# Performance work log

Hardware: AMD Instinct MI355X
Metric: run time of the kernel (lower is better)

The kernel has to match this reference:

```python
import jax, jax.numpy as jnp
import numpy as np

N_NODES, EMB, HID, HEADS, E = 50000, 128, 64, 3, 800000


def setup_inputs() -> dict:
    key = jax.random.key(0)
    ks = jax.random.split(key, 12)
    HC = HEADS * HID
    return {
        "edge_index": jax.random.randint(ks[0], (2, E), 0, N_NODES),
        "edge_attr": jax.random.uniform(ks[1], (E, 1), dtype=jnp.float32),
        "path_emb": jax.random.normal(ks[2], (N_NODES, EMB), dtype=jnp.float32) * (2.0 / EMB) ** 0.5,
        "sim_w": jnp.ones((1,), dtype=jnp.float32),
        "Wl": jax.random.normal(ks[3], (HC, EMB), dtype=jnp.float32) / np.sqrt(EMB),
        "bl": jnp.zeros((HC,), dtype=jnp.float32),
        "Wr": jax.random.normal(ks[4], (HC, EMB), dtype=jnp.float32) / np.sqrt(EMB),
        "br": jnp.zeros((HC,), dtype=jnp.float32),
        "We": jax.random.normal(ks[5], (HC, 1), dtype=jnp.float32),
        "att": jax.random.normal(ks[6], (1, HEADS, HID), dtype=jnp.float32) / np.sqrt(HID),
        "bias_gnn": jnp.zeros((HID,), dtype=jnp.float32),
        "Wout": jax.random.normal(ks[7], (1, HID), dtype=jnp.float32) / np.sqrt(HID),
        "bout": jnp.zeros((1,), dtype=jnp.float32),
    }


def reference(edge_index, edge_attr, path_emb, sim_w, Wl, bl, Wr, br, We, att, bias_gnn, Wout, bout):
    # SimFusionModule: softmax-weighted combination over sim channels -> [E, 1]
    w = jax.nn.softmax(sim_w, axis=0)
    fused = (edge_attr * w).sum(axis=1, keepdims=True)  # [E,1]

    # GATv2Conv (concat=False, no self loops, edge_dim=1)
    xl = (path_emb @ Wl.T + bl).reshape(-1, HEADS, HID)  # source transform [N,H,C]
    xr = (path_emb @ Wr.T + br).reshape(-1, HEADS, HID)  # target transform [N,H,C]
    src, dst = edge_index[0], edge_index[1]
    xj = xl[src]                                          # [E,H,C] gathered source
    xi = xr[dst]                                          # [E,H,C] gathered target
    ef = (fused @ We.T).reshape(-1, HEADS, HID)           # [E,H,C] edge features
    m = xj + xi + ef
    a = (jax.nn.leaky_relu(m, 0.2) * att).sum(-1)         # [E,H] attention logits

    # segment softmax over incoming edges of each destination node
    amax = jax.ops.segment_max(a, dst, num_segments=N_NODES)
    aexp = jnp.exp(a - amax[dst])
    asum = jax.ops.segment_sum(aexp, dst, num_segments=N_NODES)
    alpha = aexp / asum[dst]                              # [E,H]

    out = jax.ops.segment_sum(alpha[:, :, None] * xj, dst, num_segments=N_NODES)  # [N,H,C]
    out = out.mean(axis=1) + bias_gnn                     # concat=False -> head mean, + bias

    scores = (out @ Wout.T + bout).squeeze()              # [N]
    return jax.nn.softmax(scores, axis=0)
```

## Files before the change

### kernel.cpp

```cpp
#include <hip/hip_runtime.h>
#include <cfloat>
#include <cmath>

#define NHEADS 3
#define HIDC   64
#define HCC    192
#define EMBC   128
#define WCOLS  384
#define CAP    1280
#define SCH    2048
#define SPLIT  2

typedef unsigned short bhalf;
typedef __fp16 half_t;
typedef __attribute__((ext_vector_type(2))) __fp16 h2;
typedef __attribute__((ext_vector_type(8))) short bf16x8;
typedef __attribute__((ext_vector_type(4))) float f32x4;
typedef __attribute__((ext_vector_type(2))) float f32x2;

__device__ __forceinline__ unsigned f2bf(float f) {
  unsigned u = __float_as_uint(f);
  return (u + 0x7FFFu + ((u >> 16) & 1u)) >> 16;
}
__device__ __forceinline__ unsigned h2bits(h2 v) {
  union { h2 h; unsigned u; } cv; cv.h = v; return cv.u;
}

__global__ __launch_bounds__(256) void prep_kernel(
    const float* __restrict__ Wl, const float* __restrict__ Wr,
    const float* __restrict__ bl, const float* __restrict__ br,
    const float* __restrict__ We, const float* __restrict__ att,
    bhalf* __restrict__ Wb, float* __restrict__ bfl,
    unsigned* __restrict__ weh, unsigned* __restrict__ atth,
    unsigned* __restrict__ cur, float* __restrict__ sumexp, int NB)
{
  const int BASE = WCOLS * EMBC;
  int gt = blockIdx.x * 256 + threadIdx.x;
  if (gt < BASE) {
    int c = gt >> 7, k = gt & 127;
    float v = (c < HCC) ? Wl[c * EMBC + k] : Wr[(c - HCC) * EMBC + k];
    Wb[gt] = (bhalf)f2bf(v);
  } else if (gt < BASE + 384) {
    int c = gt - BASE;
    bfl[c] = (c < HCC) ? bl[c] : br[c - HCC];
  } else if (gt < BASE + 480) {
    int i = gt - BASE - 384;
    weh[i] = h2bits(__builtin_amdgcn_cvt_pkrtz(16.f * We[2 * i], 16.f * We[2 * i + 1]));
  } else if (gt < BASE + 576) {
    int i = gt - BASE - 480;
    atth[i] = h2bits(__builtin_amdgcn_cvt_pkrtz(att[2 * i] * (1.f / 16.f),
                                                att[2 * i + 1] * (1.f / 16.f)));
  } else if (gt < BASE + 576 + NB) {
    int b = gt - BASE - 576;
    cur[b * 16] = (unsigned)(b * CAP);
  } else if (gt == BASE + 576 + NB) {
    *sumexp = 0.f;
  }
}

__global__ __launch_bounds__(256, 4) void gemmscatter_kernel(
    const float* __restrict__ pe, const bhalf* __restrict__ Wb,
    const float* __restrict__ bfl, const float* __restrict__ Wout,
    unsigned char* __restrict__ xl8, unsigned char* __restrict__ xr8,
    float* __restrict__ pj, int N,
    const int* __restrict__ ei, const float* __restrict__ ea,
    uint2* __restrict__ eb, unsigned* __restrict__ cur, int E, int NSC)
{
  __shared__ union {
    bhalf Ws[192 * 64];
    struct { unsigned lh[800]; unsigned lbase[800]; } s;
  } sm;
  const int tid = threadIdx.x;

  if ((int)blockIdx.x < NSC) {
    const int base = blockIdx.x * SCH;
    for (int i = tid; i < 800; i += 256) sm.s.lh[i] = 0;
    __syncthreads();
    unsigned packed[SCH / 256];
    #pragma unroll
    for (int i = 0; i < SCH / 256; ++i) {
      int e = base + i * 256 + tid;
      packed[i] = 0xFFFFFFFFu;
      if (e < E) {
        unsigned dst = (unsigned)ei[E + e];
        unsigned r = atomicAdd(&sm.s.lh[dst >> 6], 1u);
        packed[i] = dst | (r << 16);
      }
    }
    __syncthreads();
    for (int i = tid; i < 800; i += 256) {
      unsigned c = sm.s.lh[i];
      sm.s.lbase[i] = c ? atomicAdd(&cur[i * 16], c) : 0u;
    }
    __syncthreads();
    #pragma unroll
    for (int i = 0; i < SCH / 256; ++i) {
      int e = base + i * 256 + tid;
      if (e < E) {
        unsigned pk = packed[i];
        unsigned dst = pk & 0xFFFFu;
        unsigned slot = sm.s.lbase[dst >> 6] + (pk >> 16);
        uint2 rec;
        rec.x = (unsigned)ei[e] | (dst << 16);
        rec.y = __float_as_uint(ea[e]);
        eb[slot] = rec;
      }
    }
  } else {
    const int bid  = blockIdx.x - NSC;
    const int w    = tid >> 6;
    const int lane = tid & 63;
    const int m    = lane & 15;
    const int q    = lane >> 4;
    const int nb   = bid >> 1;
    const int half = bid & 1;
    const int node = nb * 64 + w * 16 + m;
    const size_t prow = (size_t)(node < N ? node : N - 1) * EMBC;

    bf16x8 pfrag[4];
    #pragma unroll
    for (int kt = 0; kt < 4; ++kt) {
      const float* p = pe + prow + kt * 32 + q * 8;
      float4 x = *(const float4*)p;
      float4 y = *(const float4*)(p + 4);
      union { bf16x8 v; unsigned u[4]; } uu;
      uu.u[0] = (__float_as_uint(x.x) >> 16) | (__float_as_uint(x.y) & 0xFFFF0000u);
      uu.u[1] = (__float_as_uint(x.z) >> 16) | (__float_as_uint(x.w) & 0xFFFF0000u);
      uu.u[2] = (__float_as_uint(y.x) >> 16) | (__float_as_uint(y.y) & 0xFFFF0000u);
      uu.u[3] = (__float_as_uint(y.z) >> 16) | (__float_as_uint(y.w) & 0xFFFF0000u);
      pfrag[kt] = uu.v;
    }

    f32x4 acc[12];
    #pragma unroll
    for (int t = 0; t < 12; ++t) acc[t] = (f32x4){0.f, 0.f, 0.f, 0.f};

    for (int kh = 0; kh < 2; ++kh) {
      __syncthreads();
      for (int f = tid; f < 192 * 8; f += 256) {
        int cc = f >> 3, s = f & 7;
        uint4 v = *(const uint4*)(Wb + (size_t)(half * HCC + cc) * EMBC + kh * 64 + s * 8);
        *(uint4*)(sm.Ws + cc * 64 + ((s ^ (cc & 7)) * 8)) = v;
      }
      __syncthreads();
      #pragma unroll
      for (int kt2 = 0; kt2 < 2; ++kt2) {
        #pragma unroll
        for (int t = 0; t < 12; ++t) {
          bf16x8 wf = *(const bf16x8*)(sm.Ws + (t * 16 + m) * 64 + (((kt2 << 2) + q) ^ (m & 7)) * 8);
          acc[t] = __builtin_amdgcn_mfma_f32_16x16x32_bf16(wf, pfrag[kh * 2 + kt2], acc[t], 0, 0, 0);
        }
      }
    }

    float4 wo4[4];
    #pragma unroll
    for (int tt = 0; tt < 4; ++tt)
      wo4[tt] = *(const float4*)(Wout + tt * 16 + q * 4);
    float pjp[3] = {0.f, 0.f, 0.f};
    unsigned char* xo = half ? xr8 : xl8;
    #pragma unroll
    for (int t = 0; t < 12; ++t) {
      int col = t * 16 + q * 4;
      float4 b = *(const float4*)(bfl + half * HCC + col);
      float r0 = acc[t][0] + b.x;
      float r1 = acc[t][1] + b.y;
      float r2 = acc[t][2] + b.z;
      float r3 = acc[t][3] + b.w;
      if (half == 0) {
        float4 wo = wo4[t & 3];
        pjp[t >> 2] += r0 * wo.x + r1 * wo.y + r2 * wo.z + r3 * wo.w;
      }
      if (node < N) {
        int p = 0;
        p = __builtin_amdgcn_cvt_pk_fp8_f32(16.f * r0, 16.f * r1, p, false);
        p = __builtin_amdgcn_cvt_pk_fp8_f32(16.f * r2, 16.f * r3, p, true);
        *(unsigned*)(xo + (size_t)node * HCC + col) = (unsigned)p;
      }
    }
    if (half == 0) {
      #pragma unroll
      for (int h = 0; h < 3; ++h) {
        pjp[h] += __shfl_xor(pjp[h], 16);
        pjp[h] += __shfl_xor(pjp[h], 32);
      }
      if (q == 0 && node < N) {
        pj[node * 3 + 0] = pjp[0];
        pj[node * 3 + 1] = pjp[1];
        pj[node * 3 + 2] = pjp[2];
      }
    }
  }
}

#define EPG 5
#define GPW 4
#define WCHUNK (EPG * GPW)
__global__ __launch_bounds__(256, 4) void edge_kernel(
    const uint2* __restrict__ eb,
    const unsigned char* __restrict__ xl8, const unsigned char* __restrict__ xr8,
    const float* __restrict__ pj, const unsigned* __restrict__ weh,
    const unsigned* __restrict__ atth, const unsigned* __restrict__ cur,
    float* __restrict__ pfacc, int N)
{
  __shared__ float facc[64][8];
  const int tid  = threadIdx.x;
  const int w    = tid >> 6;
  const int lane = tid & 63;
  const int j = lane / 12;
  const int c = lane % 12;
  const bool act = lane < 60;
  const int cc = act ? c : 0;
  const int blk    = blockIdx.x;
  const int bucket = blk >> 1;
  const int sl     = blk & 1;
  const int start = bucket * CAP;
  const int end   = (int)cur[bucket * 16];

  for (int i = tid; i < 512; i += 256) ((float*)facc)[i] = 0.f;

  union U8 { uint4 u[2]; h2 h[8]; };
  U8 we, at;
  we.u[0] = *(const uint4*)(weh + cc * 8);
  we.u[1] = *(const uint4*)(weh + cc * 8 + 4);
  at.u[0] = *(const uint4*)(atth + cc * 8);
  at.u[1] = *(const uint4*)(atth + cc * 8 + 4);
  const h2 c02 = {(__fp16)0.2f, (__fp16)0.2f};
  __syncthreads();

  const int gw = sl * 4 + w;
  const int wstart = start + gw * WCHUNK;
  uint2 rec[GPW];
  #pragma unroll
  for (int g = 0; g < GPW; ++g) {
    int e = wstart + g * EPG + j;
    rec[g] = eb[e < end ? e : start];
  }

  for (int cb = wstart; cb < end; cb += 8 * WCHUNK) {
    int srcs[GPW], dsts[GPW]; float eavs[GPW];
    #pragma unroll
    for (int g = 0; g < GPW; ++g) {
      srcs[g] = (int)(rec[g].x & 0xFFFFu);
      dsts[g] = (int)(rec[g].x >> 16);
      eavs[g] = __uint_as_float(rec[g].y);
    }
    uint4 ul[GPW], ur[GPW]; float pjv[GPW];
    #pragma unroll
    for (int g = 0; g < GPW; ++g)
      ul[g] = *(const uint4*)(xl8 + (size_t)srcs[g] * HCC + cc * 16);
    #pragma unroll
    for (int g = 0; g < GPW; ++g)
      ur[g] = *(const uint4*)(xr8 + (size_t)dsts[g] * HCC + cc * 16);
    #pragma unroll
    for (int g = 0; g < GPW; ++g)
      pjv[g] = pj[srcs[g] * 3 + (c >> 2)];

    int nxt = cb + 8 * WCHUNK;
    #pragma unroll
    for (int g = 0; g < GPW; ++g) {
      int e = nxt + g * EPG + j;
      rec[g] = eb[(e < end) ? e : start];
    }

    #pragma unroll
    for (int g = 0; g < GPW; ++g) {
      const unsigned* ulp = &ul[g].x;
      const unsigned* urp = &ur[g].x;
      h2 eav2 = __builtin_amdgcn_cvt_pkrtz(eavs[g], eavs[g]);
      float sc = 0.f;
      #pragma unroll
      for (int i = 0; i < 4; ++i) {
        f32x2 la = __builtin_amdgcn_cvt_pk_f32_fp8(ulp[i], false);
        f32x2 lb = __builtin_amdgcn_cvt_pk_f32_fp8(ulp[i], true);
        f32x2 ra = __builtin_amdgcn_cvt_pk_f32_fp8(urp[i], false);
        f32x2 rb = __builtin_amdgcn_cvt_pk_f32_fp8(urp[i], true);
        h2 l0 = __builtin_amdgcn_cvt_pkrtz(la.x, la.y);
        h2 l1 = __builtin_amdgcn_cvt_pkrtz(lb.x, lb.y);
        h2 r0 = __builtin_amdgcn_cvt_pkrtz(ra.x, ra.y);
        h2 r1 = __builtin_amdgcn_cvt_pkrtz(rb.x, rb.y);
        h2 m0 = l0 + r0 + eav2 * we.h[2 * i];
        h2 m1 = l1 + r1 + eav2 * we.h[2 * i + 1];
        h2 q0 = __builtin_elementwise_max(m0, m0 * c02);
        h2 q1 = __builtin_elementwise_max(m1, m1 * c02);
        sc = __builtin_amdgcn_fdot2(q0, at.h[2 * i], sc, false);
        sc = __builtin_amdgcn_fdot2(q1, at.h[2 * i + 1], sc, false);
      }
      sc += __shfl_xor(sc, 1);
      sc += __shfl_xor(sc, 2);
      bool ve = act && (cb + g * EPG + j < end);
      if (ve && (c & 3) == 0) {
        int h = c >> 2;
        int ld = dsts[g] & 63;
        float ex = __expf(sc);
        atomicAdd(&facc[ld][h], ex);
        atomicAdd(&facc[ld][3 + h], ex * pjv[g]);
      }
    }
  }
  __syncthreads();

  for (int i = tid; i < 512; i += 256)
    pfacc[(size_t)blk * 512 + i] = ((float*)facc)[i];
}

__global__ __launch_bounds__(256) void finalize_kernel(
    const float* __restrict__ pfacc, float* __restrict__ sumexp,
    float* __restrict__ out, int N)
{
  int n = blockIdx.x * 256 + threadIdx.x;
  int t = threadIdx.x;
  float e = 0.f;
  if (n < N) {
    int bucket = n >> 6, ld = n & 63;
    float a0 = 0.f, a1 = 0.f, a2 = 0.f, m0 = 0.f, m1 = 0.f, m2 = 0.f;
    #pragma unroll
    for (int s = 0; s < SPLIT; ++s) {
      const float* p = pfacc + ((size_t)(bucket * SPLIT + s) * 512) + ld * 8;
      a0 += p[0]; a1 += p[1]; a2 += p[2];
      m0 += p[3]; m1 += p[4]; m2 += p[5];
    }
    float accs = 0.f;
    if (a0 > 0.f) accs += m0 / a0;
    if (a1 > 0.f) accs += m1 / a1;
    if (a2 > 0.f) accs += m2 / a2;
    e = expf(accs * (1.f / 3.f));
    out[n] = e;
  }
  __shared__ float red[256];
  red[t] = e;
  __syncthreads();
  for (int w = 128; w; w >>= 1) {
    if (t < w) red[t] += red[t + w];
    __syncthreads();
  }
  if (t == 0) atomicAdd(sumexp, red[0]);
}

__global__ __launch_bounds__(256) void norm_kernel(
    float* __restrict__ out, const float* __restrict__ sumexp, int N)
{
  int n = blockIdx.x * 256 + threadIdx.x;
  if (n < N) out[n] /= *sumexp;
}

extern "C" void kernel_launch(void* const* d_in, const int* in_sizes, int n_in,
                              void* d_out, int out_size, void* d_ws, size_t ws_size,
                              hipStream_t stream) {
  const int*   ei   = (const int*)  d_in[0];
  const float* ea   = (const float*)d_in[1];
  const float* pe   = (const float*)d_in[2];
  const float* Wl   = (const float*)d_in[4];
  const float* bl   = (const float*)d_in[5];
  const float* Wr   = (const float*)d_in[6];
  const float* br   = (const float*)d_in[7];
  const float* We   = (const float*)d_in[8];
  const float* att  = (const float*)d_in[9];
  const float* Wout = (const float*)d_in[11];

  const int E = in_sizes[0] / 2;
  const int N = in_sizes[2] / EMBC;
  const int NB = (N + 63) >> 6;
  float* out = (float*)d_out;

  float* ws       = (float*)d_ws;
  float* sumexp   = ws;
  unsigned* cur   = (unsigned*)(ws + 16);
  float* pj       = ws + 16 + (size_t)NB * 16;
  float* bfl      = pj + (size_t)3 * N;
  unsigned* weh   = (unsigned*)(bfl + 384);
  unsigned* atth  = weh + 96;
  bhalf* Wb       = (bhalf*)(atth + 96);
  unsigned char* xl8 = (unsigned char*)(Wb + (size_t)WCOLS * EMBC);
  unsigned char* xr8 = xl8 + (size_t)N * HCC;
  uint2* eb       = (uint2*)(xr8 + (size_t)N * HCC);
  float* pfacc    = (float*)(eb + (size_t)NB * CAP);

  const int BASE = WCOLS * EMBC;
  const int NSC = (E + SCH - 1) / SCH;
  prep_kernel<<<(BASE + 576 + NB + 1 + 255) / 256, 256, 0, stream>>>(
      Wl, Wr, bl, br, We, att, Wb, bfl, weh, atth, cur, sumexp, NB);
  gemmscatter_kernel<<<NSC + NB * 2, 256, 0, stream>>>(
      pe, Wb, bfl, Wout, xl8, xr8, pj, N, ei, ea, eb, cur, E, NSC);
  edge_kernel<<<NB * SPLIT, 256, 0, stream>>>(eb, xl8, xr8, pj, weh, atth,
                                              cur, pfacc, N);
  finalize_kernel<<<(N + 255) / 256, 256, 0, stream>>>(pfacc, sumexp, out, N);
  norm_kernel<<<(N + 255) / 256, 256, 0, stream>>>(out, sumexp, N);
}
```

Measured before the change: 197.9 us.

## Load GEMM weight fragments directly from global memory and double scatter chunk size

```diff
diff --git a/kernel.cpp b/kernel.cpp
--- a/kernel.cpp
+++ b/kernel.cpp
@@ -8,7 +8,7 @@
 #define EMBC   128
 #define WCOLS  384
 #define CAP    1280
-#define SCH    2048
+#define SCH    4096
 #define SPLIT  2
 
 typedef unsigned short bhalf;
@@ -66,15 +66,12 @@
     const int* __restrict__ ei, const float* __restrict__ ea,
     uint2* __restrict__ eb, unsigned* __restrict__ cur, int E, int NSC)
 {
-  __shared__ union {
-    bhalf Ws[192 * 64];
-    struct { unsigned lh[800]; unsigned lbase[800]; } s;
-  } sm;
+  __shared__ struct { unsigned lh[800]; unsigned lbase[800]; } sm;
   const int tid = threadIdx.x;
 
   if ((int)blockIdx.x < NSC) {
     const int base = blockIdx.x * SCH;
-    for (int i = tid; i < 800; i += 256) sm.s.lh[i] = 0;
+    for (int i = tid; i < 800; i += 256) sm.lh[i] = 0;
     __syncthreads();
     unsigned packed[SCH / 256];
     #pragma unroll
@@ -83,14 +80,14 @@
       packed[i] = 0xFFFFFFFFu;
       if (e < E) {
         unsigned dst = (unsigned)ei[E + e];
-        unsigned r = atomicAdd(&sm.s.lh[dst >> 6], 1u);
+        unsigned r = atomicAdd(&sm.lh[dst >> 6], 1u);
         packed[i] = dst | (r << 16);
       }
     }
     __syncthreads();
     for (int i = tid; i < 800; i += 256) {
-      unsigned c = sm.s.lh[i];
-      sm.s.lbase[i] = c ? atomicAdd(&cur[i * 16], c) : 0u;
+      unsigned c = sm.lh[i];
+      sm.lbase[i] = c ? atomicAdd(&cur[i * 16], c) : 0u;
     }
     __syncthreads();
     #pragma unroll
@@ -99,7 +96,7 @@
       if (e < E) {
         unsigned pk = packed[i];
         unsigned dst = pk & 0xFFFFu;
-        unsigned slot = sm.s.lbase[dst >> 6] + (pk >> 16);
+        unsigned slot = sm.lbase[dst >> 6] + (pk >> 16);
         uint2 rec;
         rec.x = (unsigned)ei[e] | (dst << 16);
         rec.y = __float_as_uint(ea[e]);
@@ -135,20 +132,22 @@
     #pragma unroll
     for (int t = 0; t < 12; ++t) acc[t] = (f32x4){0.f, 0.f, 0.f, 0.f};
 
+    const bhalf* Wh = Wb + (size_t)half * HCC * EMBC;
+    #pragma unroll
     for (int kh = 0; kh < 2; ++kh) {
-      __syncthreads();
-      for (int f = tid; f < 192 * 8; f += 256) {
-        int cc = f >> 3, s = f & 7;
-        uint4 v = *(const uint4*)(Wb + (size_t)(half * HCC + cc) * EMBC + kh * 64 + s * 8);
-        *(uint4*)(sm.Ws + cc * 64 + ((s ^ (cc & 7)) * 8)) = v;
-      }
-      __syncthreads();
       #pragma unroll
       for (int kt2 = 0; kt2 < 2; ++kt2) {
+        const bhalf* Wc = Wh + kh * 64 + (size_t)((kt2 << 2) + q) * 8;
         #pragma unroll
-        for (int t = 0; t < 12; ++t) {
-          bf16x8 wf = *(const bf16x8*)(sm.Ws + (t * 16 + m) * 64 + (((kt2 << 2) + q) ^ (m & 7)) * 8);
-          acc[t] = __builtin_amdgcn_mfma_f32_16x16x32_bf16(wf, pfrag[kh * 2 + kt2], acc[t], 0, 0, 0);
+        for (int tb = 0; tb < 2; ++tb) {
+          bf16x8 wf[6];
+          #pragma unroll
+          for (int t = 0; t < 6; ++t)
+            wf[t] = *(const bf16x8*)(Wc + (size_t)((tb * 6 + t) * 16 + m) * EMBC);
+          #pragma unroll
+          for (int t = 0; t < 6; ++t)
+            acc[tb * 6 + t] = __builtin_amdgcn_mfma_f32_16x16x32_bf16(
+                wf[t], pfrag[kh * 2 + kt2], acc[tb * 6 + t], 0, 0, 0);
         }
       }
     }
```

Result: slower. 212.8 us (+7.5%).
